# Optimization experiments

Hardware: AMD Instinct MI355X
Metric: run time of the kernel (lower is better)

Reference implementation:

```python
import jax, jax.numpy as jnp
import numpy as np

B, C_IN, T, N = 16, 64, 12, 5000
C_OUT = 64


def setup_inputs() -> dict:
    key = jax.random.key(0)
    k1, k2, k3, k4 = jax.random.split(key, 4)
    x = jax.random.normal(k1, (B, C_IN, T, N), dtype=jnp.float32)
    # normalized adjacency / graph shift operator (dense representation of the sparse filter)
    gcnconv_filter = jax.random.uniform(k2, (N, N), dtype=jnp.float32)
    weight = jax.random.normal(k3, (C_IN, C_OUT), dtype=jnp.float32) * (1.0 / np.sqrt(C_IN))
    bias = jax.random.normal(k4, (C_OUT,), dtype=jnp.float32) * 0.1
    return {"x": x, "gcnconv_filter": gcnconv_filter, "weight": weight, "bias": bias}


def reference(x, gcnconv_filter, weight, bias):
    batch_size, c_in, t, n_vertex = x.shape
    c_out = weight.shape[1]
    # faithful to torch: raw row-major reshape of [B, c_in, T, N] to [-1, c_in]
    x_flat = x.reshape(-1, c_in)                      # [B*T*N, c_in]
    h = (x_flat @ weight).reshape(n_vertex, -1)       # [N, B*T*c_out] (raw reshape)
    agg = gcnconv_filter @ h                          # spmm aggregation over vertices
    out = agg.reshape(-1, c_out) + bias               # [N*B*T, c_out]
    return out
```

## Files before the change

### kernel.cpp

```cpp
#include <hip/hip_runtime.h>

#define N_VERT 5000
#define NCOL   12288
#define KPAD   5056
#define MPAD   5120

#define G1_BLOCKS  15168
#define CVT_BLOCKS 25280

typedef float          f32x4  __attribute__((ext_vector_type(4)));
typedef unsigned short u16x4  __attribute__((ext_vector_type(4)));
typedef __bf16         bf16x8 __attribute__((ext_vector_type(8)));

__device__ __forceinline__ unsigned short f2bf(float f) {
  unsigned int u = __builtin_bit_cast(unsigned int, f);
  u += 0x7fffu + ((u >> 16) & 1u);
  return (unsigned short)(u >> 16);
}

__device__ __forceinline__ void async16(const unsigned short* g, unsigned short* l) {
  __builtin_amdgcn_global_load_lds(
      (const __attribute__((address_space(1))) unsigned int*)g,
      (__attribute__((address_space(3))) unsigned int*)l, 16, 0, 0);
}

__global__ __launch_bounds__(256) void prep(const float* __restrict__ x,
                                            const float* __restrict__ W,
                                            const float* __restrict__ F,
                                            unsigned short* __restrict__ Ht,
                                            unsigned short* __restrict__ Fb) {
  __shared__ float xt[64][68];
  __shared__ float Wl[64][68];
  const int tid = threadIdx.x;

  if (blockIdx.x >= G1_BLOCKS) {
    int idx = (blockIdx.x - G1_BLOCKS) * 256 + tid;
    int row = idx / (KPAD / 4);
    int c4  = (idx % (KPAD / 4)) * 4;
    u16x4 o;
    if (row < N_VERT && c4 < N_VERT) {
      f32x4 v = *(const f32x4*)(F + (long)row * N_VERT + c4);
      o.x = f2bf(v.x); o.y = f2bf(v.y); o.z = f2bf(v.z); o.w = f2bf(v.w);
    } else {
      o.x = 0; o.y = 0; o.z = 0; o.w = 0;
    }
    *(u16x4*)(Fb + (long)row * KPAD + c4) = o;
    return;
  }

  const int utile = blockIdx.x % 79;
  const int rr    = blockIdx.x / 79;

  for (int i = tid; i < 4096; i += 256) Wl[i >> 6][i & 63] = W[i];
  {
    int rowu = tid >> 2;
    int cb   = (tid & 3) * 16;
    long u   = (long)utile * 64 + rowu;
    bool valid = (u < N_VERT);
    const float* src = x + (u * 192 + rr) * 64;
#pragma unroll
    for (int q = 0; q < 4; ++q) {
      int col = cb + q * 4;
      f32x4 v = {0.f, 0.f, 0.f, 0.f};
      if (valid) v = *(const f32x4*)(src + col);
      xt[col + 0][rowu] = v.x;
      xt[col + 1][rowu] = v.y;
      xt[col + 2][rowu] = v.z;
      xt[col + 3][rowu] = v.w;
    }
  }
  __syncthreads();

  const int ul0 = (tid & 15) * 4;
  const int j0  = (tid >> 4) * 4;
  float acc[4][4] = {};
#pragma unroll 8
  for (int c = 0; c < 64; ++c) {
    f32x4 xv = *(const f32x4*)&xt[c][ul0];
    f32x4 wv = *(const f32x4*)&Wl[c][j0];
#pragma unroll
    for (int a = 0; a < 4; ++a)
#pragma unroll
      for (int b = 0; b < 4; ++b) acc[a][b] += xv[a] * wv[b];
  }

  long ug = (long)utile * 64 + ul0;
#pragma unroll
  for (int b = 0; b < 4; ++b) {
    long rowh = (long)rr * 64 + (j0 + b);
    u16x4 o = {f2bf(acc[0][b]), f2bf(acc[1][b]), f2bf(acc[2][b]), f2bf(acc[3][b])};
    *(u16x4*)(Ht + rowh * KPAD + ug) = o;
  }
}

__global__ __launch_bounds__(512, 2) void gemm2(const unsigned short* __restrict__ A,
                                                const unsigned short* __restrict__ Bt,
                                                const float* __restrict__ bias,
                                                float* __restrict__ out) {
  __shared__ __align__(16) unsigned short smem[65536];
  char* sm = (char*)smem;

  const int tid = threadIdx.x;
  const int l   = tid & 63;
  const int w   = tid >> 6;
  const int wr  = w >> 2;
  const int wc  = w & 3;
  const int la  = l & 15;

  const int xcd = blockIdx.x & 7;
  const int ii  = blockIdx.x >> 3;
  const int gg  = ii / 30;
  const int rmap= ii % 30;
  const long tM = (long)(gg * 5 + (rmap % 5)) * 256;
  const long tN = (long)(xcd * 6 + (rmap / 5)) * 256;

  const int sChunk = (l & 3) ^ ((l >> 3) & 3);
  const unsigned short* gA2 = A  + (tM + (l >> 2)) * (size_t)KPAD + sChunk * 8;
  const unsigned short* gB2 = Bt + (tN + (l >> 2)) * (size_t)KPAD + sChunk * 8;

  auto stage = [&](int bufB, const unsigned short* gA, const unsigned short* gB) {
    async16(gA + (size_t)(w * 16)       * KPAD, (unsigned short*)(sm + bufB + w * 1024));
    async16(gA + (size_t)(w * 16 + 128) * KPAD, (unsigned short*)(sm + bufB + 8192 + w * 1024));
    async16(gB + (size_t)(w * 16)       * KPAD, (unsigned short*)(sm + bufB + 16384 + w * 1024));
    async16(gB + (size_t)(w * 16 + 128) * KPAD, (unsigned short*)(sm + bufB + 16384 + 8192 + w * 1024));
  };

  const int chunkoff = ((l >> 4) ^ ((la >> 1) & 3)) << 4;
  const int aOff = (wr * 128 + la) * 64 + chunkoff;
  const int bOff = 16384 + (wc * 64 + la) * 64 + chunkoff;

  f32x4  acc[8][4] = {};
  bf16x8 af[8], bb[4];

#define BAR  __builtin_amdgcn_s_barrier()
#define SFEN __builtin_amdgcn_sched_barrier(0)

  auto region = [&](int b, int mode) {
    const char* bufp = sm + b * 32768;
    af[0] = *(const bf16x8*)(bufp + aOff);
#pragma unroll
    for (int n = 0; n < 4; ++n) bb[n] = *(const bf16x8*)(bufp + bOff + n * 1024);
#pragma unroll
    for (int m = 1; m < 8; ++m) af[m] = *(const bf16x8*)(bufp + aOff + m * 1024);
    if (mode == 0) {
      stage(((b + 3) & 3) * 32768, gA2, gB2);
      gA2 += 32; gB2 += 32;
    }
    __builtin_amdgcn_s_setprio(1);
#pragma unroll
    for (int m = 0; m < 8; ++m)
#pragma unroll
      for (int n = 0; n < 4; ++n)
        acc[m][n] = __builtin_amdgcn_mfma_f32_16x16x32_bf16(
            af[m], bb[n], acc[m][n], 0, 0, 0);
    __builtin_amdgcn_s_setprio(0);
    if (mode == 0)      { asm volatile("s_waitcnt vmcnt(8)" ::: "memory"); }
    else if (mode == 1) { asm volatile("s_waitcnt vmcnt(4)" ::: "memory"); }
    else if (mode == 2) { asm volatile("s_waitcnt vmcnt(0)" ::: "memory"); }
    if (mode != 3) { BAR; SFEN; }
  };

  stage(0,     gA2, gB2); gA2 += 32; gB2 += 32;
  stage(32768, gA2, gB2); gA2 += 32; gB2 += 32;
  stage(65536, gA2, gB2); gA2 += 32; gB2 += 32;
  asm volatile("s_waitcnt vmcnt(8)" ::: "memory");
  BAR; SFEN;

#pragma unroll 1
  for (int it = 0; it < 38; ++it) {
    region(0, 0); region(1, 0); region(2, 0); region(3, 0);
  }
  region(0, 0);
  region(1, 0);
  region(2, 0);
  region(3, 1);
  region(0, 2);
  region(1, 3);

  float bv[4];
#pragma unroll
  for (int n = 0; n < 4; ++n) bv[n] = bias[n * 16 + la];
  const int rb = (l >> 4) * 4;
#pragma unroll
  for (int m = 0; m < 8; ++m) {
    long gm0 = tM + wr * 128 + m * 16 + rb;
#pragma unroll
    for (int rr2 = 0; rr2 < 4; ++rr2) {
      long gm = gm0 + rr2;
      if (gm < N_VERT) {
#pragma unroll
        for (int n = 0; n < 4; ++n) {
          long gn = tN + wc * 64 + n * 16 + la;
          out[gm * NCOL + gn] = acc[m][n][rr2] + bv[n];
        }
      }
    }
  }
#undef BAR
#undef SFEN
}

extern "C" void kernel_launch(void* const* d_in, const int* in_sizes, int n_in,
                              void* d_out, int out_size, void* d_ws, size_t ws_size,
                              hipStream_t stream) {
  const float* x    = (const float*)d_in[0];
  const float* F    = (const float*)d_in[1];
  const float* W    = (const float*)d_in[2];
  const float* bias = (const float*)d_in[3];
  float* out = (float*)d_out;

  const size_t fbB = (size_t)MPAD * KPAD * 2;
  const size_t htB = (size_t)NCOL * KPAD * 2;
  if (ws_size < fbB + htB) return;

  unsigned short* Fb = (unsigned short*)d_ws;
  unsigned short* Ht = (unsigned short*)((char*)d_ws + fbB);

  prep <<<dim3(G1_BLOCKS + CVT_BLOCKS), 256, 0, stream>>>(x, W, F, Ht, Fb);
  gemm2<<<dim3(960),                    512, 0, stream>>>(Fb, Ht, bias, out);
}
```

Baseline: 701.6 us.

## Pre-swizzle H into MFMA fragment layout and load B operands directly to registers

```diff
diff --git a/kernel.cpp b/kernel.cpp
--- a/kernel.cpp
+++ b/kernel.cpp
@@ -87,9 +87,11 @@
   long ug = (long)utile * 64 + ul0;
 #pragma unroll
   for (int b = 0; b < 4; ++b) {
-    long rowh = (long)rr * 64 + (j0 + b);
+    long col = (long)rr * 64 + (j0 + b);
     u16x4 o = {f2bf(acc[0][b]), f2bf(acc[1][b]), f2bf(acc[2][b]), f2bf(acc[3][b])};
-    *(u16x4*)(Ht + rowh * KPAD + ug) = o;
+    long idx = (col >> 4) * (long)(KPAD * 16)
+             + (ug >> 5) * 512 + ((ug >> 3) & 3) * 128 + (col & 15) * 8 + (ug & 7);
+    *(u16x4*)(Ht + idx) = o;
   }
 }
 
@@ -114,68 +116,85 @@
   const long tM = (long)(gg * 5 + (rmap % 5)) * 256;
   const long tN = (long)(xcd * 6 + (rmap / 5)) * 256;
 
-  const int sChunk = (l & 3) ^ ((l >> 3) & 3);
-  const unsigned short* gA2 = A  + (tM + (l >> 2)) * (size_t)KPAD + sChunk * 8;
-  const unsigned short* gB2 = Bt + (tN + (l >> 2)) * (size_t)KPAD + sChunk * 8;
-
-  auto stage = [&](int bufB, const unsigned short* gA, const unsigned short* gB) {
-    async16(gA + (size_t)(w * 16)       * KPAD, (unsigned short*)(sm + bufB + w * 1024));
-    async16(gA + (size_t)(w * 16 + 128) * KPAD, (unsigned short*)(sm + bufB + 8192 + w * 1024));
-    async16(gB + (size_t)(w * 16)       * KPAD, (unsigned short*)(sm + bufB + 16384 + w * 1024));
-    async16(gB + (size_t)(w * 16 + 128) * KPAD, (unsigned short*)(sm + bufB + 16384 + 8192 + w * 1024));
+  const int  sRow  = l >> 3;
+  const int  sCol8 = ((l & 7) ^ (l >> 3)) * 8;
+  const unsigned short* gA2 = A + (tM + sRow) * (size_t)KPAD + sCol8;
+
+  auto stageA = [&](int bufB, const unsigned short* g) {
+    async16(g + (size_t)(w * 8)       * KPAD, (unsigned short*)(sm + bufB + w * 1024));
+    async16(g + (size_t)(w * 8 + 64)  * KPAD, (unsigned short*)(sm + bufB + (w + 8) * 1024));
+    async16(g + (size_t)(w * 8 + 128) * KPAD, (unsigned short*)(sm + bufB + 16384 + w * 1024));
+    async16(g + (size_t)(w * 8 + 192) * KPAD, (unsigned short*)(sm + bufB + 16384 + (w + 8) * 1024));
   };
 
-  const int chunkoff = ((l >> 4) ^ ((la >> 1) & 3)) << 4;
-  const int aOff = (wr * 128 + la) * 64 + chunkoff;
-  const int bOff = 16384 + (wc * 64 + la) * 64 + chunkoff;
+  const int cOff0 = ((l >> 4) * 16)      ^ ((l & 7) << 4);
+  const int cOff1 = (64 + (l >> 4) * 16) ^ ((l & 7) << 4);
+  const int aRow  = (wr * 128 + la) * 128;
+  const char* pa0 = sm + aRow + cOff0;
+  const char* pa1 = sm + aRow + cOff1;
+
+  const size_t KB16 = (size_t)KPAD * 16;
+  const unsigned short* gB = Bt + ((size_t)(tN >> 4) + wc * 4) * KB16 + l * 8;
 
   f32x4  acc[8][4] = {};
-  bf16x8 af[8], bb[4];
-
-#define BAR  __builtin_amdgcn_s_barrier()
-#define SFEN __builtin_amdgcn_sched_barrier(0)
-
-  auto region = [&](int b, int mode) {
-    const char* bufp = sm + b * 32768;
-    af[0] = *(const bf16x8*)(bufp + aOff);
-#pragma unroll
-    for (int n = 0; n < 4; ++n) bb[n] = *(const bf16x8*)(bufp + bOff + n * 1024);
-#pragma unroll
-    for (int m = 1; m < 8; ++m) af[m] = *(const bf16x8*)(bufp + aOff + m * 1024);
-    if (mode == 0) {
-      stage(((b + 3) & 3) * 32768, gA2, gB2);
-      gA2 += 32; gB2 += 32;
-    }
+  bf16x8 af[8], ag[8], B0[4], B1[4];
+  int kb = 0;
+
+  auto tile = [&](int bi, int mode) {
+    const char* a0 = pa0 + bi * 32768;
+    const char* a1 = pa1 + bi * 32768;
+#pragma unroll
+    for (int m = 0; m < 8; ++m) af[m] = *(const bf16x8*)(a0 + m * 2048);
+#pragma unroll
+    for (int m = 0; m < 8; ++m) ag[m] = *(const bf16x8*)(a1 + m * 2048);
+#pragma unroll
+    for (int n = 0; n < 4; ++n) B1[n] = *(const bf16x8*)(gB + n * KB16 + kb + 512);
+    if (mode == 0) { stageA(((bi + 3) & 3) * 32768, gA2); gA2 += 64; }
     __builtin_amdgcn_s_setprio(1);
 #pragma unroll
     for (int m = 0; m < 8; ++m)
 #pragma unroll
       for (int n = 0; n < 4; ++n)
-        acc[m][n] = __builtin_amdgcn_mfma_f32_16x16x32_bf16(
-            af[m], bb[n], acc[m][n], 0, 0, 0);
+        acc[m][n] = __builtin_amdgcn_mfma_f32_16x16x32_bf16(af[m], B0[n], acc[m][n], 0, 0, 0);
     __builtin_amdgcn_s_setprio(0);
-    if (mode == 0)      { asm volatile("s_waitcnt vmcnt(8)" ::: "memory"); }
-    else if (mode == 1) { asm volatile("s_waitcnt vmcnt(4)" ::: "memory"); }
-    else if (mode == 2) { asm volatile("s_waitcnt vmcnt(0)" ::: "memory"); }
-    if (mode != 3) { BAR; SFEN; }
+    if (mode != 3) {
+#pragma unroll
+      for (int n = 0; n < 4; ++n) B0[n] = *(const bf16x8*)(gB + n * KB16 + kb + 1024);
+    }
+    __builtin_amdgcn_s_setprio(1);
+#pragma unroll
+    for (int m = 0; m < 8; ++m)
+#pragma unroll
+      for (int n = 0; n < 4; ++n)
+        acc[m][n] = __builtin_amdgcn_mfma_f32_16x16x32_bf16(ag[m], B1[n], acc[m][n], 0, 0, 0);
+    __builtin_amdgcn_s_setprio(0);
+    kb += 1024;
+    if (mode == 0)      { asm volatile("s_waitcnt vmcnt(24)" ::: "memory"); }
+    else if (mode == 1) { asm volatile("s_waitcnt vmcnt(20)" ::: "memory"); }
+    else if (mode == 2) { asm volatile("s_waitcnt vmcnt(16)" ::: "memory"); }
+    if (mode != 3) {
+      __builtin_amdgcn_s_barrier();
+      __builtin_amdgcn_sched_barrier(0);
+    }
   };
 
-  stage(0,     gA2, gB2); gA2 += 32; gB2 += 32;
-  stage(32768, gA2, gB2); gA2 += 32; gB2 += 32;
-  stage(65536, gA2, gB2); gA2 += 32; gB2 += 32;
-  asm volatile("s_waitcnt vmcnt(8)" ::: "memory");
-  BAR; SFEN;
+  stageA(0,     gA2);
+  stageA(32768, gA2 + 64);
+  stageA(65536, gA2 + 128);
+  gA2 += 192;
+  asm volatile("s_waitcnt vmcnt(0)" ::: "memory");
+#pragma unroll
+  for (int n = 0; n < 4; ++n) B0[n] = *(const bf16x8*)(gB + n * KB16);
+  __builtin_amdgcn_s_barrier();
+  __builtin_amdgcn_sched_barrier(0);
 
 #pragma unroll 1
-  for (int it = 0; it < 38; ++it) {
-    region(0, 0); region(1, 0); region(2, 0); region(3, 0);
-  }
-  region(0, 0);
-  region(1, 0);
-  region(2, 0);
-  region(3, 1);
-  region(0, 2);
-  region(1, 3);
+  for (int it = 0; it < 19; ++it) {
+    tile(0, 0); tile(1, 0); tile(2, 0); tile(3, 0);
+  }
+  tile(0, 1);
+  tile(1, 2);
+  tile(2, 3);
 
   float bv[4];
 #pragma unroll
@@ -196,8 +215,6 @@
       }
     }
   }
-#undef BAR
-#undef SFEN
 }
 
 extern "C" void kernel_launch(void* const* d_in, const int* in_sizes, int n_in,
```

After: 823.0 us. +17.3%, slower.
